# Kernel tuning notes

Measured on AMD Instinct MI355X. Metric: run time of the kernel, lower is better.

## Reference

```python
import jax, jax.numpy as jnp
import numpy as np
import math

FREQS = jnp.array([1., 2., 4., 8., 7., 5.], dtype=jnp.float32)  # default frequencies


def setup_inputs() -> dict:
    key = jax.random.key(0)
    k1, k2, k3 = jax.random.split(key, 3)
    B, N, H, F = 8, 4096, 256, 6
    x = jax.random.normal(k1, (B, N, H), dtype=jnp.float32)
    t = jax.random.uniform(k2, (B, 1), dtype=jnp.float32) * (2.0 * math.pi)
    oscillators = jax.random.normal(k3, (F, H, H), dtype=jnp.float32) * 0.1
    # phase_shifts[i] = i / F * pi, broadcast over hidden dim (matches torch init)
    phase_shifts = jnp.broadcast_to(
        (jnp.arange(F, dtype=jnp.float32) / F * math.pi)[:, None], (F, H)
    ).copy()
    return {"x": x, "t": t, "oscillators": oscillators, "phase_shifts": phase_shifts}


def reference(x, t, oscillators, phase_shifts):
    # resonator[b, f, h] = sin(freq_f * t[b, 0] + phase[f, h])
    res = jnp.sin(FREQS[None, :, None] * t[:, :, None] + phase_shifts[None, :, :])  # [B, F, H]
    # result[b, n, k] = sum_f (x[b, n, :] @ W_f)[k] * res[b, f, k]
    return jnp.einsum('bnh,fhk,bfk->bnk', x, oscillators, res)
```

## Files before the change

kernel.cpp:

```cpp
#include <hip/hip_runtime.h>
#include <hip/hip_bf16.h>


#define B_  8
#define N_  4096
#define H_  256

typedef __attribute__((ext_vector_type(8))) short s8v;
typedef __attribute__((ext_vector_type(4))) float f4v;

__global__ __launch_bounds__(256) void build_w(
    const float* __restrict__ osc,
    const float* __restrict__ t,
    const float* __restrict__ phase,
    __hip_bfloat16* __restrict__ Wt)
{
    const float freqs[6] = {1.f, 2.f, 4.f, 8.f, 7.f, 5.f};
    __shared__ float tr[16 * 68];

    const int b  = blockIdx.z;
    const int n0 = blockIdx.y * 64;
    const int h0 = blockIdx.x * 128;
    const int tid = threadIdx.x;

    const float tb = t[b];
    const int nr = (tid & 15) * 4;
    const int hr = tid >> 4;
    float s[6][4];
#pragma unroll
    for (int f = 0; f < 6; ++f)
#pragma unroll
        for (int j = 0; j < 4; ++j)
            s[f][j] = __sinf(freqs[f] * tb + phase[f * 256 + n0 + nr + j]);

    const int nw = tid >> 2;
    const int hw = (tid & 3) * 4;
    __hip_bfloat16* wout = Wt + (size_t)b * 65536 + (size_t)(n0 + nw) * 256 + h0;

    for (int hp = 0; hp < 8; ++hp) {
        const int h = h0 + hp * 16 + hr;
        float4 acc = make_float4(0.f, 0.f, 0.f, 0.f);
#pragma unroll
        for (int f = 0; f < 6; ++f) {
            float4 o = *(const float4*)&osc[f * 65536 + h * 256 + n0 + nr];
            acc.x += o.x * s[f][0];
            acc.y += o.y * s[f][1];
            acc.z += o.z * s[f][2];
            acc.w += o.w * s[f][3];
        }
        __syncthreads();
        *(float4*)&tr[hr * 68 + nr] = acc;
        __syncthreads();
        float v0 = tr[(hw + 0) * 68 + nw];
        float v1 = tr[(hw + 1) * 68 + nw];
        float v2 = tr[(hw + 2) * 68 + nw];
        float v3 = tr[(hw + 3) * 68 + nw];
        union { __hip_bfloat162 h2[2]; unsigned long long q; } cv;
        cv.h2[0] = __float22bfloat162_rn(make_float2(v0, v1));
        cv.h2[1] = __float22bfloat162_rn(make_float2(v2, v3));
        *(unsigned long long*)(wout + hp * 16 + hw) = cv.q;
    }
}

#define LDST 72

__global__ __launch_bounds__(512, 4) void gemm(
    const float* __restrict__ X,
    const __hip_bfloat16* __restrict__ Wt,
    float* __restrict__ out)
{
    __shared__ short As[64 * LDST];
    __shared__ short Bs[256 * LDST];

    const int b     = blockIdx.y;
    const int mTile = blockIdx.x;

    const int tid    = threadIdx.x;
    const int lane   = tid & 63;
    const int wave   = tid >> 6;
    const int lane15 = lane & 15;
    const int quad   = lane >> 4;
    const int wm     = wave >> 2;
    const int wn     = wave & 3;

    const float* Xb          = X   + (size_t)b * N_ * H_ + (size_t)mTile * 64 * H_;
    const __hip_bfloat16* Wb = Wt  + (size_t)b * H_ * H_;
    float* Ob                = out + (size_t)b * N_ * H_ + (size_t)mTile * 64 * H_;

    const int arow = tid >> 3;
    const int aseg = (tid & 7) * 8;
    const float* pa = Xb + (size_t)arow * H_ + aseg;

    const int brow = tid >> 1;
    const int bhf  = (tid & 1) * 32;
    const __hip_bfloat16* pb = Wb + (size_t)brow * H_ + bhf;

    f4v acc[2][4] = {};

    float4 a0 = *(const float4*)pa;
    float4 a1 = *(const float4*)(pa + 4);
    uint4  bv0 = *(const uint4*)(pb);
    uint4  bv1 = *(const uint4*)(pb + 8);
    uint4  bv2 = *(const uint4*)(pb + 16);
    uint4  bv3 = *(const uint4*)(pb + 24);

    for (int it = 0; it < 4; ++it) {
        union { __hip_bfloat162 h2[4]; uint4 q; } cv;
        cv.h2[0] = __float22bfloat162_rn(make_float2(a0.x, a0.y));
        cv.h2[1] = __float22bfloat162_rn(make_float2(a0.z, a0.w));
        cv.h2[2] = __float22bfloat162_rn(make_float2(a1.x, a1.y));
        cv.h2[3] = __float22bfloat162_rn(make_float2(a1.z, a1.w));
        *(uint4*)(&As[arow * LDST + aseg]) = cv.q;
        *(uint4*)(&Bs[brow * LDST + bhf + 0])  = bv0;
        *(uint4*)(&Bs[brow * LDST + bhf + 8])  = bv1;
        *(uint4*)(&Bs[brow * LDST + bhf + 16]) = bv2;
        *(uint4*)(&Bs[brow * LDST + bhf + 24]) = bv3;
        __syncthreads();

        if (it < 3) {
            const int k = (it + 1) * 64;
            a0  = *(const float4*)(pa + k);
            a1  = *(const float4*)(pa + k + 4);
            bv0 = *(const uint4*)(pb + k);
            bv1 = *(const uint4*)(pb + k + 8);
            bv2 = *(const uint4*)(pb + k + 16);
            bv3 = *(const uint4*)(pb + k + 24);
        }

#pragma unroll
        for (int kh = 0; kh < 2; ++kh) {
            s8v af[2], bf[4];
#pragma unroll
            for (int mt = 0; mt < 2; ++mt)
                af[mt] = *(const s8v*)(&As[(wm * 32 + mt * 16 + lane15) * LDST + kh * 32 + quad * 8]);
#pragma unroll
            for (int nt = 0; nt < 4; ++nt)
                bf[nt] = *(const s8v*)(&Bs[(wn * 64 + nt * 16 + lane15) * LDST + kh * 32 + quad * 8]);
#pragma unroll
            for (int mt = 0; mt < 2; ++mt)
#pragma unroll
                for (int nt = 0; nt < 4; ++nt)
                    acc[mt][nt] = __builtin_amdgcn_mfma_f32_16x16x32_bf16(
                        af[mt], bf[nt], acc[mt][nt], 0, 0, 0);
        }
        __syncthreads();
    }

#pragma unroll
    for (int mt = 0; mt < 2; ++mt) {
#pragma unroll
        for (int r = 0; r < 4; ++r) {
            int row = wm * 32 + mt * 16 + quad * 4 + r;
            float* po = Ob + (size_t)row * H_ + wn * 64 + lane15;
#pragma unroll
            for (int nt = 0; nt < 4; ++nt)
                __builtin_nontemporal_store(acc[mt][nt][r], po + nt * 16);
        }
    }
}

extern "C" void kernel_launch(void* const* d_in, const int* in_sizes, int n_in,
                              void* d_out, int out_size, void* d_ws, size_t ws_size,
                              hipStream_t stream) {
    const float* x     = (const float*)d_in[0];
    const float* t     = (const float*)d_in[1];
    const float* osc   = (const float*)d_in[2];
    const float* phase = (const float*)d_in[3];
    __hip_bfloat16* Wt = (__hip_bfloat16*)d_ws;
    float* out = (float*)d_out;

    dim3 gw(2, 4, 8);
    build_w<<<gw, 256, 0, stream>>>(osc, t, phase, Wt);

    dim3 gg(64, 8);
    gemm<<<gg, 512, 0, stream>>>(x, Wt, out);
}
```

Before: 97.25 us.

## Split build_w and gemm into smaller tiles to launch more blocks

build_w now gives each block a single 16-wide h slice and drops its inner loop over h, so the grid goes from 64 to 512 blocks. The GEMM M tile shrinks from 64 to 32 rows, doubling the grid to 1024 blocks, and the launch-bounds occupancy hint is raised from 4 to 6. The goal is to fill more of the GPU's compute units on this memory-bound problem. In exchange, every GEMM block reloads the full 256x256 W tile from L2 for half as many output rows, and each wave does half as many MFMAs per LDS load.

```diff
diff --git a/kernel.cpp b/kernel.cpp
--- a/kernel.cpp
+++ b/kernel.cpp
@@ -20,7 +20,7 @@
 
     const int b  = blockIdx.z;
     const int n0 = blockIdx.y * 64;
-    const int h0 = blockIdx.x * 128;
+    const int h0 = blockIdx.x * 16;
     const int tid = threadIdx.x;
 
     const float tb = t[b];
@@ -33,43 +33,39 @@
         for (int j = 0; j < 4; ++j)
             s[f][j] = __sinf(freqs[f] * tb + phase[f * 256 + n0 + nr + j]);
 
+    const int h = h0 + hr;
+    float4 acc = make_float4(0.f, 0.f, 0.f, 0.f);
+#pragma unroll
+    for (int f = 0; f < 6; ++f) {
+        float4 o = *(const float4*)&osc[f * 65536 + h * 256 + n0 + nr];
+        acc.x += o.x * s[f][0];
+        acc.y += o.y * s[f][1];
+        acc.z += o.z * s[f][2];
+        acc.w += o.w * s[f][3];
+    }
+    *(float4*)&tr[hr * 68 + nr] = acc;
+    __syncthreads();
+
     const int nw = tid >> 2;
     const int hw = (tid & 3) * 4;
-    __hip_bfloat16* wout = Wt + (size_t)b * 65536 + (size_t)(n0 + nw) * 256 + h0;
-
-    for (int hp = 0; hp < 8; ++hp) {
-        const int h = h0 + hp * 16 + hr;
-        float4 acc = make_float4(0.f, 0.f, 0.f, 0.f);
-#pragma unroll
-        for (int f = 0; f < 6; ++f) {
-            float4 o = *(const float4*)&osc[f * 65536 + h * 256 + n0 + nr];
-            acc.x += o.x * s[f][0];
-            acc.y += o.y * s[f][1];
-            acc.z += o.z * s[f][2];
-            acc.w += o.w * s[f][3];
-        }
-        __syncthreads();
-        *(float4*)&tr[hr * 68 + nr] = acc;
-        __syncthreads();
-        float v0 = tr[(hw + 0) * 68 + nw];
-        float v1 = tr[(hw + 1) * 68 + nw];
-        float v2 = tr[(hw + 2) * 68 + nw];
-        float v3 = tr[(hw + 3) * 68 + nw];
-        union { __hip_bfloat162 h2[2]; unsigned long long q; } cv;
-        cv.h2[0] = __float22bfloat162_rn(make_float2(v0, v1));
-        cv.h2[1] = __float22bfloat162_rn(make_float2(v2, v3));
-        *(unsigned long long*)(wout + hp * 16 + hw) = cv.q;
-    }
+    float v0 = tr[(hw + 0) * 68 + nw];
+    float v1 = tr[(hw + 1) * 68 + nw];
+    float v2 = tr[(hw + 2) * 68 + nw];
+    float v3 = tr[(hw + 3) * 68 + nw];
+    union { __hip_bfloat162 h2[2]; unsigned long long q; } cv;
+    cv.h2[0] = __float22bfloat162_rn(make_float2(v0, v1));
+    cv.h2[1] = __float22bfloat162_rn(make_float2(v2, v3));
+    *(unsigned long long*)(Wt + (size_t)b * 65536 + (size_t)(n0 + nw) * 256 + h0 + hw) = cv.q;
 }
 
 #define LDST 72
 
-__global__ __launch_bounds__(512, 4) void gemm(
+__global__ __launch_bounds__(512, 6) void gemm(
     const float* __restrict__ X,
     const __hip_bfloat16* __restrict__ Wt,
     float* __restrict__ out)
 {
-    __shared__ short As[64 * LDST];
+    __shared__ short As[32 * LDST];
     __shared__ short Bs[256 * LDST];
 
     const int b     = blockIdx.y;
@@ -83,34 +79,31 @@
     const int wm     = wave >> 2;
     const int wn     = wave & 3;
 
-    const float* Xb          = X   + (size_t)b * N_ * H_ + (size_t)mTile * 64 * H_;
+    const float* Xb          = X   + (size_t)b * N_ * H_ + (size_t)mTile * 32 * H_;
     const __hip_bfloat16* Wb = Wt  + (size_t)b * H_ * H_;
-    float* Ob                = out + (size_t)b * N_ * H_ + (size_t)mTile * 64 * H_;
+    float* Ob                = out + (size_t)b * N_ * H_ + (size_t)mTile * 32 * H_;
 
-    const int arow = tid >> 3;
-    const int aseg = (tid & 7) * 8;
+    const int arow = tid >> 4;
+    const int aseg = (tid & 15) * 4;
     const float* pa = Xb + (size_t)arow * H_ + aseg;
 
     const int brow = tid >> 1;
     const int bhf  = (tid & 1) * 32;
     const __hip_bfloat16* pb = Wb + (size_t)brow * H_ + bhf;
 
-    f4v acc[2][4] = {};
+    f4v acc[4] = {};
 
-    float4 a0 = *(const float4*)pa;
-    float4 a1 = *(const float4*)(pa + 4);
+    float4 av  = *(const float4*)pa;
     uint4  bv0 = *(const uint4*)(pb);
     uint4  bv1 = *(const uint4*)(pb + 8);
     uint4  bv2 = *(const uint4*)(pb + 16);
     uint4  bv3 = *(const uint4*)(pb + 24);
 
     for (int it = 0; it < 4; ++it) {
-        union { __hip_bfloat162 h2[4]; uint4 q; } cv;
-        cv.h2[0] = __float22bfloat162_rn(make_float2(a0.x, a0.y));
-        cv.h2[1] = __float22bfloat162_rn(make_float2(a0.z, a0.w));
-        cv.h2[2] = __float22bfloat162_rn(make_float2(a1.x, a1.y));
-        cv.h2[3] = __float22bfloat162_rn(make_float2(a1.z, a1.w));
-        *(uint4*)(&As[arow * LDST + aseg]) = cv.q;
+        union { __hip_bfloat162 h2[2]; unsigned long long q; } cv;
+        cv.h2[0] = __float22bfloat162_rn(make_float2(av.x, av.y));
+        cv.h2[1] = __float22bfloat162_rn(make_float2(av.z, av.w));
+        *(unsigned long long*)(&As[arow * LDST + aseg]) = cv.q;
         *(uint4*)(&Bs[brow * LDST + bhf + 0])  = bv0;
         *(uint4*)(&Bs[brow * LDST + bhf + 8])  = bv1;
         *(uint4*)(&Bs[brow * LDST + bhf + 16]) = bv2;
@@ -119,8 +112,7 @@
 
         if (it < 3) {
             const int k = (it + 1) * 64;
-            a0  = *(const float4*)(pa + k);
-            a1  = *(const float4*)(pa + k + 4);
+            av  = *(const float4*)(pa + k);
             bv0 = *(const uint4*)(pb + k);
             bv1 = *(const uint4*)(pb + k + 8);
             bv2 = *(const uint4*)(pb + k + 16);
@@ -129,33 +121,26 @@
 
 #pragma unroll
         for (int kh = 0; kh < 2; ++kh) {
-            s8v af[2], bf[4];
-#pragma unroll
-            for (int mt = 0; mt < 2; ++mt)
-                af[mt] = *(const s8v*)(&As[(wm * 32 + mt * 16 + lane15) * LDST + kh * 32 + quad * 8]);
+            s8v af, bf[4];
+            af = *(const s8v*)(&As[(wm * 16 + lane15) * LDST + kh * 32 + quad * 8]);
 #pragma unroll
             for (int nt = 0; nt < 4; ++nt)
                 bf[nt] = *(const s8v*)(&Bs[(wn * 64 + nt * 16 + lane15) * LDST + kh * 32 + quad * 8]);
 #pragma unroll
-            for (int mt = 0; mt < 2; ++mt)
-#pragma unroll
-                for (int nt = 0; nt < 4; ++nt)
-                    acc[mt][nt] = __builtin_amdgcn_mfma_f32_16x16x32_bf16(
-                        af[mt], bf[nt], acc[mt][nt], 0, 0, 0);
+            for (int nt = 0; nt < 4; ++nt)
+                acc[nt] = __builtin_amdgcn_mfma_f32_16x16x32_bf16(
+                    af, bf[nt], acc[nt], 0, 0, 0);
         }
         __syncthreads();
     }
 
 #pragma unroll
-    for (int mt = 0; mt < 2; ++mt) {
+    for (int r = 0; r < 4; ++r) {
+        int row = wm * 16 + quad * 4 + r;
+        float* po = Ob + (size_t)row * H_ + wn * 64 + lane15;
 #pragma unroll
-        for (int r = 0; r < 4; ++r) {
-            int row = wm * 32 + mt * 16 + quad * 4 + r;
-            float* po = Ob + (size_t)row * H_ + wn * 64 + lane15;
-#pragma unroll
-            for (int nt = 0; nt < 4; ++nt)
-                __builtin_nontemporal_store(acc[mt][nt][r], po + nt * 16);
-        }
+        for (int nt = 0; nt < 4; ++nt)
+            __builtin_nontemporal_store(acc[nt][r], po + nt * 16);
     }
 }
 
@@ -169,9 +154,9 @@
     __hip_bfloat16* Wt = (__hip_bfloat16*)d_ws;
     float* out = (float*)d_out;
 
-    dim3 gw(2, 4, 8);
+    dim3 gw(16, 4, 8);
     build_w<<<gw, 256, 0, stream>>>(osc, t, phase, Wt);
 
-    dim3 gg(64, 8);
+    dim3 gg(128, 8);
     gemm<<<gg, 512, 0, stream>>>(x, Wt, out);
 }
```

New measurement: 98.37 us. Within noise of the previous version (+1.2%).

## Parallelize weight build across more blocks and double-buffer GEMM global prefetch

Applied to the files above, without the earlier changes.

build_w now launches 8x more blocks, each handling a single 16-row h slice, which removes the per-block loop and its repeated barriers. The GEMM prefetches two K-slices of X and W into registers up front, so global loads run two stages ahead. __syncthreads is replaced with an inline-asm barrier that waits only on LDS counters, so in-flight global loads no longer stall the barrier. This costs more registers for the second prefetch slot, and the hand-written barrier depends on the compiler not reordering memory operations around it.

```diff
diff --git a/kernel.cpp b/kernel.cpp
--- a/kernel.cpp
+++ b/kernel.cpp
@@ -8,6 +8,8 @@
 
 typedef __attribute__((ext_vector_type(8))) short s8v;
 typedef __attribute__((ext_vector_type(4))) float f4v;
+
+#define LGK_BARRIER() asm volatile("s_waitcnt lgkmcnt(0)\n\ts_barrier" ::: "memory")
 
 __global__ __launch_bounds__(256) void build_w(
     const float* __restrict__ osc,
@@ -20,7 +22,7 @@
 
     const int b  = blockIdx.z;
     const int n0 = blockIdx.y * 64;
-    const int h0 = blockIdx.x * 128;
+    const int h0 = blockIdx.x * 16;
     const int tid = threadIdx.x;
 
     const float tb = t[b];
@@ -33,33 +35,29 @@
         for (int j = 0; j < 4; ++j)
             s[f][j] = __sinf(freqs[f] * tb + phase[f * 256 + n0 + nr + j]);
 
+    const int h = h0 + hr;
+    float4 acc = make_float4(0.f, 0.f, 0.f, 0.f);
+#pragma unroll
+    for (int f = 0; f < 6; ++f) {
+        float4 o = *(const float4*)&osc[f * 65536 + h * 256 + n0 + nr];
+        acc.x += o.x * s[f][0];
+        acc.y += o.y * s[f][1];
+        acc.z += o.z * s[f][2];
+        acc.w += o.w * s[f][3];
+    }
+    *(float4*)&tr[hr * 68 + nr] = acc;
+    __syncthreads();
+
     const int nw = tid >> 2;
     const int hw = (tid & 3) * 4;
-    __hip_bfloat16* wout = Wt + (size_t)b * 65536 + (size_t)(n0 + nw) * 256 + h0;
-
-    for (int hp = 0; hp < 8; ++hp) {
-        const int h = h0 + hp * 16 + hr;
-        float4 acc = make_float4(0.f, 0.f, 0.f, 0.f);
-#pragma unroll
-        for (int f = 0; f < 6; ++f) {
-            float4 o = *(const float4*)&osc[f * 65536 + h * 256 + n0 + nr];
-            acc.x += o.x * s[f][0];
-            acc.y += o.y * s[f][1];
-            acc.z += o.z * s[f][2];
-            acc.w += o.w * s[f][3];
-        }
-        __syncthreads();
-        *(float4*)&tr[hr * 68 + nr] = acc;
-        __syncthreads();
-        float v0 = tr[(hw + 0) * 68 + nw];
-        float v1 = tr[(hw + 1) * 68 + nw];
-        float v2 = tr[(hw + 2) * 68 + nw];
-        float v3 = tr[(hw + 3) * 68 + nw];
-        union { __hip_bfloat162 h2[2]; unsigned long long q; } cv;
-        cv.h2[0] = __float22bfloat162_rn(make_float2(v0, v1));
-        cv.h2[1] = __float22bfloat162_rn(make_float2(v2, v3));
-        *(unsigned long long*)(wout + hp * 16 + hw) = cv.q;
-    }
+    float v0 = tr[(hw + 0) * 68 + nw];
+    float v1 = tr[(hw + 1) * 68 + nw];
+    float v2 = tr[(hw + 2) * 68 + nw];
+    float v3 = tr[(hw + 3) * 68 + nw];
+    union { __hip_bfloat162 h2[2]; unsigned long long q; } cv;
+    cv.h2[0] = __float22bfloat162_rn(make_float2(v0, v1));
+    cv.h2[1] = __float22bfloat162_rn(make_float2(v2, v3));
+    *(unsigned long long*)(Wt + (size_t)b * 65536 + (size_t)(n0 + nw) * 256 + h0 + hw) = cv.q;
 }
 
 #define LDST 72
@@ -97,34 +95,39 @@
 
     f4v acc[2][4] = {};
 
-    float4 a0 = *(const float4*)pa;
-    float4 a1 = *(const float4*)(pa + 4);
-    uint4  bv0 = *(const uint4*)(pb);
-    uint4  bv1 = *(const uint4*)(pb + 8);
-    uint4  bv2 = *(const uint4*)(pb + 16);
-    uint4  bv3 = *(const uint4*)(pb + 24);
+    float4 a0[2], a1[2];
+    uint4  bv[2][4];
+#pragma unroll
+    for (int sl = 0; sl < 2; ++sl) {
+        const int k = sl * 64;
+        a0[sl] = *(const float4*)(pa + k);
+        a1[sl] = *(const float4*)(pa + k + 4);
+#pragma unroll
+        for (int j = 0; j < 4; ++j)
+            bv[sl][j] = *(const uint4*)(pb + k + j * 8);
+    }
 
     for (int it = 0; it < 4; ++it) {
+        const int sl = it & 1;
         union { __hip_bfloat162 h2[4]; uint4 q; } cv;
-        cv.h2[0] = __float22bfloat162_rn(make_float2(a0.x, a0.y));
-        cv.h2[1] = __float22bfloat162_rn(make_float2(a0.z, a0.w));
-        cv.h2[2] = __float22bfloat162_rn(make_float2(a1.x, a1.y));
-        cv.h2[3] = __float22bfloat162_rn(make_float2(a1.z, a1.w));
+        cv.h2[0] = __float22bfloat162_rn(make_float2(a0[sl].x, a0[sl].y));
+        cv.h2[1] = __float22bfloat162_rn(make_float2(a0[sl].z, a0[sl].w));
+        cv.h2[2] = __float22bfloat162_rn(make_float2(a1[sl].x, a1[sl].y));
+        cv.h2[3] = __float22bfloat162_rn(make_float2(a1[sl].z, a1[sl].w));
         *(uint4*)(&As[arow * LDST + aseg]) = cv.q;
-        *(uint4*)(&Bs[brow * LDST + bhf + 0])  = bv0;
-        *(uint4*)(&Bs[brow * LDST + bhf + 8])  = bv1;
-        *(uint4*)(&Bs[brow * LDST + bhf + 16]) = bv2;
-        *(uint4*)(&Bs[brow * LDST + bhf + 24]) = bv3;
-        __syncthreads();
+        *(uint4*)(&Bs[brow * LDST + bhf + 0])  = bv[sl][0];
+        *(uint4*)(&Bs[brow * LDST + bhf + 8])  = bv[sl][1];
+        *(uint4*)(&Bs[brow * LDST + bhf + 16]) = bv[sl][2];
+        *(uint4*)(&Bs[brow * LDST + bhf + 24]) = bv[sl][3];
+        LGK_BARRIER();
 
-        if (it < 3) {
-            const int k = (it + 1) * 64;
-            a0  = *(const float4*)(pa + k);
-            a1  = *(const float4*)(pa + k + 4);
-            bv0 = *(const uint4*)(pb + k);
-            bv1 = *(const uint4*)(pb + k + 8);
-            bv2 = *(const uint4*)(pb + k + 16);
-            bv3 = *(const uint4*)(pb + k + 24);
+        if (it < 2) {
+            const int k = (it + 2) * 64;
+            a0[sl] = *(const float4*)(pa + k);
+            a1[sl] = *(const float4*)(pa + k + 4);
+#pragma unroll
+            for (int j = 0; j < 4; ++j)
+                bv[sl][j] = *(const uint4*)(pb + k + j * 8);
         }
 
 #pragma unroll
@@ -143,7 +146,7 @@
                     acc[mt][nt] = __builtin_amdgcn_mfma_f32_16x16x32_bf16(
                         af[mt], bf[nt], acc[mt][nt], 0, 0, 0);
         }
-        __syncthreads();
+        LGK_BARRIER();
     }
 
 #pragma unroll
@@ -169,7 +172,7 @@
     __hip_bfloat16* Wt = (__hip_bfloat16*)d_ws;
     float* out = (float*)d_out;
 
-    dim3 gw(2, 4, 8);
+    dim3 gw(16, 4, 8);
     build_w<<<gw, 256, 0, stream>>>(osc, t, phase, Wt);
 
     dim3 gg(64, 8);
```

Result: faster. 94.06 us (-3.3%).
